# Performance work log

Measured on AMD Instinct MI355X. Metric: run time of the kernel, lower is better.

## Reference

```python
import jax, jax.numpy as jnp
import numpy as np

EMBED_DIM = 1024
HEADS = 16
D_K = EMBED_DIM // HEADS
B, S = 2, 2048


def setup_inputs() -> dict:
    key = jax.random.key(0)
    ks = jax.random.split(key, 8)
    scale = 1.0 / np.sqrt(EMBED_DIM)
    inp = {
        "key": jax.random.normal(ks[0], (B, S, EMBED_DIM), dtype=jnp.float32),
        "query": jax.random.normal(ks[1], (B, S, EMBED_DIM), dtype=jnp.float32),
        "value": jax.random.normal(ks[2], (B, S, EMBED_DIM), dtype=jnp.float32),
        # torch nn.Linear stores weight as [out, in]; y = x @ W.T
        "Wq": jax.random.normal(ks[3], (EMBED_DIM, EMBED_DIM), dtype=jnp.float32) * scale,
        "Wk": jax.random.normal(ks[4], (EMBED_DIM, EMBED_DIM), dtype=jnp.float32) * scale,
        "Wv": jax.random.normal(ks[5], (EMBED_DIM, EMBED_DIM), dtype=jnp.float32) * scale,
        "Wo": jax.random.normal(ks[6], (EMBED_DIM, EMBED_DIM), dtype=jnp.float32) * scale,
        "bo": jax.random.normal(ks[7], (EMBED_DIM,), dtype=jnp.float32) * scale,
        # causal mask, True = keep (matches masked_fill(~mask, -1e20))
        "mask": jnp.tril(jnp.ones((S, S), dtype=jnp.bool_))[None, None, :, :],
    }
    return inp


def _split_heads(x):
    b, s, _ = x.shape
    return x.reshape(b, s, HEADS, D_K).transpose(0, 2, 1, 3)  # [B,H,S,d_k]


def reference(key, query, value, Wq, Wk, Wv, Wo, bo, mask):
    b, q_len = query.shape[0], query.shape[1]
    k = _split_heads(key @ Wk.T)
    q = _split_heads(query @ Wq.T)
    v = _split_heads(value @ Wv.T)
    scores = jnp.einsum('bhqd,bhkd->bhqk', q, k) / np.sqrt(D_K)
    scores = jnp.where(mask, scores, jnp.float32(-1e20))
    attn = jax.nn.softmax(scores, axis=-1)
    out = jnp.einsum('bhqk,bhkd->bhqd', attn, v)
    out = out.transpose(0, 2, 1, 3).reshape(b, q_len, HEADS * D_K)
    return out @ Wo.T + bo
```

## Files before the change

### kernel.cpp

```cpp
#include <hip/hip_runtime.h>
#include <cstdint>
#include <cstddef>


typedef __bf16 bf16;
typedef __bf16 bf16x4 __attribute__((ext_vector_type(4)));
typedef __bf16 bf16x8 __attribute__((ext_vector_type(8)));
typedef float f32x4 __attribute__((ext_vector_type(4)));

#define MFMA(a, b, c) __builtin_amdgcn_mfma_f32_16x16x32_bf16(a, b, c, 0, 0, 0)

constexpr int EMBED = 1024;
constexpr int SEQ = 2048;
constexpr int HEADS = 16;
constexpr int DK = 64;
constexpr int BH = 32;

__device__ __forceinline__ void gl16(const bf16* g, bf16* l) {
  __builtin_amdgcn_global_load_lds(
      (const __attribute__((address_space(1))) unsigned int*)g,
      (__attribute__((address_space(3))) unsigned int*)l, 16, 0, 0);
}

struct ConvArgs {
  const void* src[8];
  bf16* dst[8];
  int n8[8];
  const unsigned short* probe;
};

__global__ __launch_bounds__(256) void convert_kernel(ConvArgs a) {
  __shared__ int cnt;
  const int t = threadIdx.x;
  if (t == 0) cnt = 0;
  __syncthreads();
  {
    unsigned short u = a.probe[2 * t];
    int e = (u >> 7) & 0xFF;
    if (e >= 100 && e <= 130) atomicAdd(&cnt, 1);
  }
  __syncthreads();
  const int isf32 = (cnt < 128) ? 1 : 0;

  const int seg = blockIdx.y;
  const void* s = a.src[seg];
  bf16* d = a.dst[seg];
  const int n8 = a.n8[seg];
  for (int i = blockIdx.x * 256 + t; i < n8; i += gridDim.x * 256) {
    if (isf32) {
      const float* sp = (const float*)s + (size_t)i * 8;
      float4 x = *(const float4*)sp, y = *(const float4*)(sp + 4);
      bf16x8 v;
      v[0] = (bf16)x.x; v[1] = (bf16)x.y; v[2] = (bf16)x.z; v[3] = (bf16)x.w;
      v[4] = (bf16)y.x; v[5] = (bf16)y.y; v[6] = (bf16)y.z; v[7] = (bf16)y.w;
      *(bf16x8*)(d + (size_t)i * 8) = v;
    } else {
      *(uint4*)(d + (size_t)i * 8) = *(const uint4*)((const bf16*)s + (size_t)i * 8);
    }
  }
}

__device__ __forceinline__ void gemm_body(
    const bf16* __restrict__ X, const bf16* __restrict__ W,
    const bf16* __restrict__ bias, bf16* __restrict__ outb,
    float* __restrict__ outf, int mode, bf16* As, bf16* Bs, int m0, int n0)
{
  const int t = threadIdx.x;
  const int lane = t & 63, wave = t >> 6;
  const int wm = wave >> 2, wn = wave & 3;
  const int l16 = lane & 15, quad = lane >> 4;

  f32x4 acc[4][2] = {};

  for (int k0 = 0; k0 < EMBED; k0 += 64) {
    __syncthreads();
#pragma unroll
    for (int i = 0; i < 2; ++i) {
      int idx = t + i * 512;
      int r = idx >> 3;
      int cl = (idx & 7) ^ (r & 7);
      gl16(X + (size_t)(m0 + r) * EMBED + k0 + cl * 8, As + (i * 512 + wave * 64) * 8);
      gl16(W + (size_t)(n0 + r) * EMBED + k0 + cl * 8, Bs + (i * 512 + wave * 64) * 8);
    }
    __syncthreads();

#pragma unroll
    for (int ks = 0; ks < 2; ++ks) {
      bf16x8 a[4], b[2];
#pragma unroll
      for (int mi = 0; mi < 4; ++mi) {
        int row = wm * 64 + mi * 16 + l16;
        a[mi] = *(const bf16x8*)(As + row * 64 + (((ks * 4 + quad) ^ (row & 7)) * 8));
      }
#pragma unroll
      for (int ni = 0; ni < 2; ++ni) {
        int row = wn * 32 + ni * 16 + l16;
        b[ni] = *(const bf16x8*)(Bs + row * 64 + (((ks * 4 + quad) ^ (row & 7)) * 8));
      }
#pragma unroll
      for (int mi = 0; mi < 4; ++mi)
#pragma unroll
        for (int ni = 0; ni < 2; ++ni)
          acc[mi][ni] = MFMA(a[mi], b[ni], acc[mi][ni]);
    }
  }

#pragma unroll
  for (int mi = 0; mi < 4; ++mi) {
#pragma unroll
    for (int ni = 0; ni < 2; ++ni) {
      int n = n0 + wn * 32 + ni * 16 + l16;
#pragma unroll
      for (int r = 0; r < 4; ++r) {
        int m = m0 + wm * 64 + mi * 16 + quad * 4 + r;
        float v = acc[mi][ni][r];
        if (mode == 2) {
          outf[(size_t)m * EMBED + n] = v + (float)bias[n];
        } else {
          int b_ = m >> 11, s = m & (SEQ - 1);
          int h = n >> 6, d = n & 63;
          int bh = b_ * HEADS + h;
          if (mode == 0)
            outb[((size_t)bh * SEQ + s) * DK + d] = (bf16)v;
          else
            outb[((size_t)bh * DK + d) * SEQ + s] = (bf16)v;
        }
      }
    }
  }
}

struct QkvArgs {
  const bf16 *X0, *X1, *X2;
  const bf16 *W0, *W1, *W2;
  bf16 *O0, *O1, *O2;
};

__global__ __launch_bounds__(512, 4) void qkv_gemm(QkvArgs args) {
  __shared__ alignas(16) bf16 As[128 * 64];
  __shared__ alignas(16) bf16 Bs[128 * 64];
  const int z = blockIdx.z;
  const bf16* X = (z == 0) ? args.X0 : (z == 1) ? args.X1 : args.X2;
  const bf16* W = (z == 0) ? args.W0 : (z == 1) ? args.W1 : args.W2;
  bf16* O      = (z == 0) ? args.O0 : (z == 1) ? args.O1 : args.O2;
  int mode = (z == 2) ? 1 : 0;
  gemm_body(X, W, nullptr, O, nullptr, mode, As, Bs,
            blockIdx.x * 128, blockIdx.y * 128);
}

__global__ __launch_bounds__(512, 4) void out_gemm(const bf16* __restrict__ X,
                                                   const bf16* __restrict__ W,
                                                   const bf16* __restrict__ bias,
                                                   float* __restrict__ out) {
  __shared__ alignas(16) bf16 As[128 * 64];
  __shared__ alignas(16) bf16 Bs[128 * 64];
  gemm_body(X, W, bias, nullptr, out, 2, As, Bs,
            blockIdx.x * 128, blockIdx.y * 128);
}

template<bool MASKED>
__device__ __forceinline__ void attn_tile2(
    int kt, int t, int w, int l16, int quad, int qbase,
    const bf16* __restrict__ Kp0, const bf16* __restrict__ Vp0,
    bf16* Ks, bf16* VTs, bf16* Pw,
    const bf16x8 qf[2][2], f32x4 o[2][4], float lst[2])
{
  constexpr float SC = 0.125f * 1.44269504f;
  constexpr float BI = -8.0f * 1.44269504f;

  __syncthreads();
  const bf16* Kg = Kp0 + (size_t)kt * 64 * DK;
  const bf16* Vg = Vp0 + (size_t)kt * 64;
#pragma unroll
  for (int i = 0; i < 2; ++i) {
    int idx = t + i * 256;
    int r = idx >> 3;
    int cl = (idx & 7) ^ (r & 7);
    gl16(Kg + (size_t)r * DK + cl * 8, Ks + (i * 256 + w * 64) * 8);
    gl16(Vg + (size_t)r * SEQ + cl * 8, VTs + (i * 256 + w * 64) * 8);
  }
  __syncthreads();

  f32x4 sacc[2][4] = {};
#pragma unroll
  for (int ks = 0; ks < 2; ++ks) {
#pragma unroll
    for (int mi = 0; mi < 4; ++mi) {
      int row = mi * 16 + l16;
      bf16x8 kf = *(const bf16x8*)(Ks + row * 64 + (((ks * 4 + quad) ^ (row & 7)) * 8));
      sacc[0][mi] = MFMA(kf, qf[0][ks], sacc[0][mi]);
      sacc[1][mi] = MFMA(kf, qf[1][ks], sacc[1][mi]);
    }
  }

#pragma unroll
  for (int g = 0; g < 2; ++g) {
    const int qg = qbase + g * 16 + l16;
    float ls = 0.f;
#pragma unroll
    for (int mi = 0; mi < 4; ++mi) {
      bf16x4 pv;
#pragma unroll
      for (int r = 0; r < 4; ++r) {
        float arg = __builtin_fmaf(sacc[g][mi][r], SC, BI);
        if (MASKED && (kt * 64 + mi * 16 + quad * 4 + r > qg)) arg = -1e30f;
        float p = __builtin_exp2f(arg);
        ls += p;
        pv[r] = (bf16)p;
      }
      *(bf16x4*)(Pw + (g * 16 + l16) * 72 + mi * 16 + quad * 4) = pv;
    }
    ls += __shfl_xor(ls, 16);
    ls += __shfl_xor(ls, 32);
    lst[g] += ls;
  }

  __builtin_amdgcn_s_setprio(1);
#pragma unroll
  for (int ks = 0; ks < 2; ++ks) {
    bf16x8 pf0 = *(const bf16x8*)(Pw + l16 * 72 + ks * 32 + quad * 8);
    bf16x8 pf1 = *(const bf16x8*)(Pw + (16 + l16) * 72 + ks * 32 + quad * 8);
#pragma unroll
    for (int dt = 0; dt < 4; ++dt) {
      int row = dt * 16 + l16;
      bf16x8 vf = *(const bf16x8*)(VTs + row * 64 +
                                   (((ks * 4 + quad) ^ (row & 7)) * 8));
      o[0][dt] = MFMA(vf, pf0, o[0][dt]);
      o[1][dt] = MFMA(vf, pf1, o[1][dt]);
    }
  }
  __builtin_amdgcn_s_setprio(0);
}

__global__ __launch_bounds__(256, 3) void attn_split(
    const bf16* __restrict__ qbuf, const bf16* __restrict__ kbuf,
    const bf16* __restrict__ vtbuf, bf16* __restrict__ ctx,
    float* __restrict__ po, float* __restrict__ pl)
{
  __shared__ alignas(16) bf16 Ks[64 * 64];
  __shared__ alignas(16) bf16 VTs[64 * 64];
  __shared__ alignas(16) bf16 Ps[4 * 32 * 72];

  const int t = threadIdx.x;
  const int gid = blockIdx.x;
  const int xcd = gid & 7, j = gid >> 3;
  const int bh = xcd + ((j & 3) << 3);
  const int s = j >> 2;
  const int mode = (s < 8) ? 0 : (s < 16) ? 1 : 2;
  const int qt = (mode == 2) ? (s - 8) : s;
  const int q0 = qt * 128;
  const int lane = t & 63, w = t >> 6;
  const int l16 = lane & 15, quad = lane >> 4;
  const int qbase = q0 + w * 32;

  const bf16* Kp0 = kbuf + (size_t)bh * SEQ * DK;
  const bf16* Vp0 = vtbuf + (size_t)bh * DK * SEQ;

  bf16x8 qf[2][2];
#pragma unroll
  for (int g = 0; g < 2; ++g) {
    const bf16* Qg = qbuf + ((size_t)bh * SEQ + qbase + g * 16 + l16) * DK;
    qf[g][0] = *(const bf16x8*)(Qg + quad * 8);
    qf[g][1] = *(const bf16x8*)(Qg + 32 + quad * 8);
  }

  float lst[2] = {0.f, 0.f};
  f32x4 o[2][4] = {};
  bf16* Pw = Ps + w * (32 * 72);

  const int t0 = (mode == 2) ? 16 : 0;
  const int tEnd = (mode == 1) ? 15 : (2 * qt - 1);
#pragma unroll 1
  for (int kt = t0; kt <= tEnd; ++kt)
    attn_tile2<false>(kt, t, w, l16, quad, qbase, Kp0, Vp0, Ks, VTs, Pw, qf, o, lst);
  if (mode != 1) {
    attn_tile2<true>(2 * qt, t, w, l16, quad, qbase, Kp0, Vp0, Ks, VTs, Pw, qf, o, lst);
    attn_tile2<true>(2 * qt + 1, t, w, l16, quad, qbase, Kp0, Vp0, Ks, VTs, Pw, qf, o, lst);
  }

  if (mode == 0) {
    const int b_ = bh >> 4, h = bh & 15;
#pragma unroll
    for (int g = 0; g < 2; ++g) {
      const float inv = 1.0f / lst[g];
      bf16* dst = ctx + ((size_t)b_ * SEQ + qbase + g * 16 + l16) * EMBED + h * DK;
#pragma unroll
      for (int dt = 0; dt < 4; ++dt) {
        bf16x4 v;
#pragma unroll
        for (int r = 0; r < 4; ++r) v[r] = (bf16)(o[g][dt][r] * inv);
        *(bf16x4*)(dst + dt * 16 + quad * 4) = v;
      }
    }
  } else {
    const int p = ((bh << 3) + (qt - 8)) * 2 + (mode - 1);
    float* ob = po + (size_t)p * 8192;
#pragma unroll
    for (int g = 0; g < 2; ++g) {
      const int qloc = w * 32 + g * 16 + l16;
#pragma unroll
      for (int dt = 0; dt < 4; ++dt)
        *(f32x4*)(ob + qloc * 64 + dt * 16 + quad * 4) = o[g][dt];
      if (quad == 0) pl[(size_t)p * 128 + qloc] = lst[g];
    }
  }
}

__global__ __launch_bounds__(256) void attn_combine(
    const float* __restrict__ po, const float* __restrict__ pl,
    bf16* __restrict__ ctx)
{
  const int gid = blockIdx.x;
  const int xcd = gid & 7, j = gid >> 3;
  const int bh = xcd + ((j & 3) << 3);
  const int qtl = j >> 2;
  const int p0 = (bh << 3) + qtl;
  const int qt = 8 + qtl;
  const int t = threadIdx.x;
  const float* o0 = po + (size_t)p0 * 2 * 8192;
  const float* o1 = o0 + 8192;
  const float* l0 = pl + (size_t)p0 * 2 * 128;
  const float* l1 = l0 + 128;

  const int q = t >> 1;
  const int d0 = (t & 1) * 32;
  const float inv = 1.0f / (l0[q] + l1[q]);

  const int b_ = bh >> 4, h = bh & 15;
  bf16* dst = ctx + ((size_t)b_ * SEQ + qt * 128 + q) * EMBED + h * DK + d0;
#pragma unroll
  for (int jj = 0; jj < 8; ++jj) {
    f32x4 a = *(const f32x4*)(o0 + q * 64 + d0 + jj * 4);
    f32x4 b = *(const f32x4*)(o1 + q * 64 + d0 + jj * 4);
    bf16x4 v;
#pragma unroll
    for (int r = 0; r < 4; ++r) v[r] = (bf16)((a[r] + b[r]) * inv);
    *(bf16x4*)(dst + jj * 4) = v;
  }
}

template<bool MASKED>
__device__ __forceinline__ void attn_tile(
    int kt, int t, int w, int l16, int quad, int qglob,
    const bf16* __restrict__ Kp0, const bf16* __restrict__ Vp0,
    bf16* Ks, bf16* VTs, bf16* Pw,
    const bf16x8 qf[2], f32x4 o[4], float& lst)
{
  constexpr float SC = 0.125f * 1.44269504f;
  constexpr float BI = -8.0f * 1.44269504f;

  __syncthreads();
  const bf16* Kg = Kp0 + (size_t)kt * 64 * DK;
  const bf16* Vg = Vp0 + (size_t)kt * 64;
#pragma unroll
  for (int i = 0; i < 2; ++i) {
    int idx = t + i * 256;
    int r = idx >> 3;
    int cl = (idx & 7) ^ (r & 7);
    gl16(Kg + (size_t)r * DK + cl * 8, Ks + (i * 256 + w * 64) * 8);
    gl16(Vg + (size_t)r * SEQ + cl * 8, VTs + (i * 256 + w * 64) * 8);
  }
  __syncthreads();

  f32x4 sacc[4] = {};
#pragma unroll
  for (int ks = 0; ks < 2; ++ks) {
#pragma unroll
    for (int mi = 0; mi < 4; ++mi) {
      int row = mi * 16 + l16;
      bf16x8 kf = *(const bf16x8*)(Ks + row * 64 + (((ks * 4 + quad) ^ (row & 7)) * 8));
      sacc[mi] = MFMA(kf, qf[ks], sacc[mi]);
    }
  }

  float ls = 0.f;
  const int kbase = kt * 64 + quad * 4;
#pragma unroll
  for (int mi = 0; mi < 4; ++mi) {
    bf16x4 pv;
#pragma unroll
    for (int r = 0; r < 4; ++r) {
      float arg = __builtin_fmaf(sacc[mi][r], SC, BI);
      if (MASKED && (kbase + mi * 16 + r > qglob)) arg = -1e30f;
      float p = __builtin_exp2f(arg);
      ls += p;
      pv[r] = (bf16)p;
    }
    *(bf16x4*)(Pw + l16 * 72 + mi * 16 + quad * 4) = pv;
  }
  ls += __shfl_xor(ls, 16);
  ls += __shfl_xor(ls, 32);
  lst += ls;

  __builtin_amdgcn_s_setprio(1);
#pragma unroll
  for (int ks = 0; ks < 2; ++ks) {
    bf16x8 pf = *(const bf16x8*)(Pw + l16 * 72 + ks * 32 + quad * 8);
#pragma unroll
    for (int dt = 0; dt < 4; ++dt) {
      int row = dt * 16 + l16;
      bf16x8 vf = *(const bf16x8*)(VTs + row * 64 +
                                   (((ks * 4 + quad) ^ (row & 7)) * 8));
      o[dt] = MFMA(vf, pf, o[dt]);
    }
  }
  __builtin_amdgcn_s_setprio(0);
}

__global__ __launch_bounds__(256, 6) void attn_mono(
    const bf16* __restrict__ qbuf, const bf16* __restrict__ kbuf,
    const bf16* __restrict__ vtbuf, bf16* __restrict__ ctx)
{
  __shared__ alignas(16) bf16 Ks[64 * 64];
  __shared__ alignas(16) bf16 VTs[64 * 64];
  __shared__ alignas(16) bf16 Ps[64 * 72];

  const int t = threadIdx.x;
  const int g = (blockIdx.x + blockIdx.y) & 31;
  const int qt = (blockIdx.y & 16) ? (31 - g) : g;
  const int bh = blockIdx.y;
  const int q0 = qt * 64;
  const int lane = t & 63, w = t >> 6;
  const int l16 = lane & 15, quad = lane >> 4;

  const bf16* Kp0 = kbuf + (size_t)bh * SEQ * DK;
  const bf16* Vp0 = vtbuf + (size_t)bh * DK * SEQ;

  const bf16* Qg = qbuf + ((size_t)bh * SEQ + q0 + w * 16 + l16) * DK;
  bf16x8 qf[2];
  qf[0] = *(const bf16x8*)(Qg + quad * 8);
  qf[1] = *(const bf16x8*)(Qg + 32 + quad * 8);

  const int qglob = q0 + w * 16 + l16;
  float lst = 0.f;
  f32x4 o[4] = {};
  bf16* Pw = Ps + w * 16 * 72;

#pragma unroll 1
  for (int kt = 0; kt < qt; ++kt)
    attn_tile<false>(kt, t, w, l16, quad, qglob, Kp0, Vp0, Ks, VTs, Pw, qf, o, lst);
  attn_tile<true>(qt, t, w, l16, quad, qglob, Kp0, Vp0, Ks, VTs, Pw, qf, o, lst);

  const float inv = 1.0f / lst;
  const int b_ = bh >> 4, h = bh & 15;
  bf16* dst = ctx + ((size_t)b_ * SEQ + qglob) * EMBED + h * DK;
#pragma unroll
  for (int dt = 0; dt < 4; ++dt) {
    bf16x4 v;
#pragma unroll
    for (int r = 0; r < 4; ++r) v[r] = (bf16)(o[dt][r] * inv);
    *(bf16x4*)(dst + dt * 16 + quad * 4) = v;
  }
}

extern "C" void kernel_launch(void* const* d_in, const int* in_sizes, int n_in,
                              void* d_out, int out_size, void* d_ws, size_t ws_size,
                              hipStream_t stream) {
  const void* key   = d_in[0];
  const void* query = d_in[1];
  const void* value = d_in[2];
  const void* Wq    = d_in[3];
  const void* Wk    = d_in[4];
  const void* Wv    = d_in[5];
  const void* Wo    = d_in[6];
  const void* bo    = d_in[7];
  float* out = (float*)d_out;

  char* base = (char*)d_ws + 256;
  const size_t XN = (size_t)2 * SEQ * EMBED;
  const size_t WN = (size_t)EMBED * EMBED;
  const size_t per = (size_t)BH * SEQ * DK;

  bf16* cq  = (bf16*)base;
  bf16* ck  = cq + XN;
  bf16* cv  = ck + XN;
  bf16* cWq = cv + XN;
  bf16* cWk = cWq + WN;
  bf16* cWv = cWk + WN;
  bf16* cWo = cWv + WN;
  bf16* cbo = cWo + WN;
  bf16* qb  = cbo + 1024;
  bf16* kb  = qb + per;
  bf16* vtb = kb + per;
  bf16* ctx = vtb + per;

  float* po = (float*)(ctx + per);
  float* pl = po + (size_t)256 * 2 * 8192;
  const size_t need = 256 + (3 * XN + 4 * WN + 1024 + 4 * per) * sizeof(bf16)
                    + (size_t)256 * 2 * 8192 * 4 + (size_t)256 * 2 * 128 * 4;
  const bool split_ok = (ws_size >= need);

  ConvArgs ca;
  ca.src[0] = query; ca.dst[0] = cq;  ca.n8[0] = (int)(XN / 8);
  ca.src[1] = key;   ca.dst[1] = ck;  ca.n8[1] = (int)(XN / 8);
  ca.src[2] = value; ca.dst[2] = cv;  ca.n8[2] = (int)(XN / 8);
  ca.src[3] = Wq;    ca.dst[3] = cWq; ca.n8[3] = (int)(WN / 8);
  ca.src[4] = Wk;    ca.dst[4] = cWk; ca.n8[4] = (int)(WN / 8);
  ca.src[5] = Wv;    ca.dst[5] = cWv; ca.n8[5] = (int)(WN / 8);
  ca.src[6] = Wo;    ca.dst[6] = cWo; ca.n8[6] = (int)(WN / 8);
  ca.src[7] = bo;    ca.dst[7] = cbo; ca.n8[7] = 128;
  ca.probe = (const unsigned short*)Wq;
  convert_kernel<<<dim3(512, 8), 256, 0, stream>>>(ca);

  QkvArgs qa{cq, ck, cv, cWq, cWk, cWv, qb, kb, vtb};
  qkv_gemm<<<dim3(32, 8, 3), 512, 0, stream>>>(qa);

  if (split_ok) {
    attn_split<<<dim3(768), 256, 0, stream>>>(qb, kb, vtb, ctx, po, pl);
    attn_combine<<<dim3(256), 256, 0, stream>>>(po, pl, ctx);
  } else {
    attn_mono<<<dim3(32, 32), 256, 0, stream>>>(qb, kb, vtb, ctx);
  }

  out_gemm<<<dim3(32, 8), 512, 0, stream>>>(ctx, cWo, cbo, out);
}
```

Measured before the change: 245.7 us.

## Use 256-row query tiles with 512 threads and multi-chunk causal KV split

The causal attention kernel now uses 512-thread blocks covering 256 query rows and splits each query tile's KV range into chunks of 8 key tiles, with up to 4 chunks per tile. Partial outputs are stored in bf16 inside the reused query conversion buffer, and the combine kernel sums a variable number of chunks. The aim is to balance causal work across blocks, halve the K/V reloads per query row, and cut partial-output traffic. In exchange, occupancy per block changes, bf16 partials lose some precision, and reusing the cq buffer assumes it is dead after the QKV GEMM.

```diff
diff --git a/kernel.cpp b/kernel.cpp
--- a/kernel.cpp
+++ b/kernel.cpp
@@ -169,15 +169,13 @@
   constexpr float BI = -8.0f * 1.44269504f;
 
   __syncthreads();
-  const bf16* Kg = Kp0 + (size_t)kt * 64 * DK;
-  const bf16* Vg = Vp0 + (size_t)kt * 64;
-#pragma unroll
-  for (int i = 0; i < 2; ++i) {
-    int idx = t + i * 256;
-    int r = idx >> 3;
-    int cl = (idx & 7) ^ (r & 7);
-    gl16(Kg + (size_t)r * DK + cl * 8, Ks + (i * 256 + w * 64) * 8);
-    gl16(Vg + (size_t)r * SEQ + cl * 8, VTs + (i * 256 + w * 64) * 8);
+  {
+    const bf16* Kg = Kp0 + (size_t)kt * 64 * DK;
+    const bf16* Vg = Vp0 + (size_t)kt * 64;
+    int r = t >> 3;
+    int cl = (t & 7) ^ (r & 7);
+    gl16(Kg + (size_t)r * DK + cl * 8, Ks + w * 512);
+    gl16(Vg + (size_t)r * SEQ + cl * 8, VTs + w * 512);
   }
   __syncthreads();
 
@@ -232,23 +230,35 @@
   __builtin_amdgcn_s_setprio(0);
 }
 
-__global__ __launch_bounds__(256, 3) void attn_split(
+__global__ __launch_bounds__(512, 6) void attn_split(
     const bf16* __restrict__ qbuf, const bf16* __restrict__ kbuf,
     const bf16* __restrict__ vtbuf, bf16* __restrict__ ctx,
-    float* __restrict__ po, float* __restrict__ pl)
+    bf16* __restrict__ po, float* __restrict__ pl)
 {
   __shared__ alignas(16) bf16 Ks[64 * 64];
   __shared__ alignas(16) bf16 VTs[64 * 64];
-  __shared__ alignas(16) bf16 Ps[4 * 32 * 72];
+  __shared__ alignas(16) bf16 Ps[8 * 32 * 72];
 
   const int t = threadIdx.x;
   const int gid = blockIdx.x;
   const int xcd = gid & 7, j = gid >> 3;
   const int bh = xcd + ((j & 3) << 3);
   const int s = j >> 2;
-  const int mode = (s < 8) ? 0 : (s < 16) ? 1 : 2;
-  const int qt = (mode == 2) ? (s - 8) : s;
-  const int q0 = qt * 128;
+
+  int qt, ch;
+  if (s < 2)       { qt = s; ch = 0; }
+  else if (s < 6)  { int u = s - 2; qt = 2 + (u >> 1); ch = u & 1; }
+  else if (s < 12) { int u = s - 6; int hi = (u >= 3) ? 1 : 0; qt = 4 + hi; ch = u - 3 * hi; }
+  else             { int u = s - 12; qt = 6 + (u >> 2); ch = u & 3; }
+
+  const int q0 = qt * 256;
+  const int t0 = ch * 8;
+  const int dEnd = 4 * qt + 3;
+  const int t1 = (t0 + 7 < dEnd) ? (t0 + 7) : dEnd;
+  const int uEnd = (t1 < 4 * qt - 1) ? t1 : (4 * qt - 1);
+  const int m0 = (t0 > 4 * qt) ? t0 : (4 * qt);
+  const bool direct = (qt < 2);
+
   const int lane = t & 63, w = t >> 6;
   const int l16 = lane & 15, quad = lane >> 4;
   const int qbase = q0 + w * 32;
@@ -268,17 +278,14 @@
   f32x4 o[2][4] = {};
   bf16* Pw = Ps + w * (32 * 72);
 
-  const int t0 = (mode == 2) ? 16 : 0;
-  const int tEnd = (mode == 1) ? 15 : (2 * qt - 1);
 #pragma unroll 1
-  for (int kt = t0; kt <= tEnd; ++kt)
+  for (int kt = t0; kt <= uEnd; ++kt)
     attn_tile2<false>(kt, t, w, l16, quad, qbase, Kp0, Vp0, Ks, VTs, Pw, qf, o, lst);
-  if (mode != 1) {
-    attn_tile2<true>(2 * qt, t, w, l16, quad, qbase, Kp0, Vp0, Ks, VTs, Pw, qf, o, lst);
-    attn_tile2<true>(2 * qt + 1, t, w, l16, quad, qbase, Kp0, Vp0, Ks, VTs, Pw, qf, o, lst);
-  }
-
-  if (mode == 0) {
+#pragma unroll 1
+  for (int kt = m0; kt <= t1; ++kt)
+    attn_tile2<true>(kt, t, w, l16, quad, qbase, Kp0, Vp0, Ks, VTs, Pw, qf, o, lst);
+
+  if (direct) {
     const int b_ = bh >> 4, h = bh & 15;
 #pragma unroll
     for (int g = 0; g < 2; ++g) {
@@ -293,49 +300,65 @@
       }
     }
   } else {
-    const int p = ((bh << 3) + (qt - 8)) * 2 + (mode - 1);
-    float* ob = po + (size_t)p * 8192;
+    const int p = ((bh * 6) + (qt - 2)) * 4 + ch;
+    bf16* ob = po + (size_t)p * 16384;
 #pragma unroll
     for (int g = 0; g < 2; ++g) {
       const int qloc = w * 32 + g * 16 + l16;
 #pragma unroll
-      for (int dt = 0; dt < 4; ++dt)
-        *(f32x4*)(ob + qloc * 64 + dt * 16 + quad * 4) = o[g][dt];
-      if (quad == 0) pl[(size_t)p * 128 + qloc] = lst[g];
+      for (int dt = 0; dt < 4; ++dt) {
+        bf16x4 v;
+#pragma unroll
+        for (int r = 0; r < 4; ++r) v[r] = (bf16)o[g][dt][r];
+        *(bf16x4*)(ob + qloc * 64 + dt * 16 + quad * 4) = v;
+      }
+      if (quad == 0) pl[(size_t)p * 256 + qloc] = lst[g];
     }
   }
 }
 
 __global__ __launch_bounds__(256) void attn_combine(
-    const float* __restrict__ po, const float* __restrict__ pl,
+    const bf16* __restrict__ po, const float* __restrict__ pl,
     bf16* __restrict__ ctx)
 {
   const int gid = blockIdx.x;
   const int xcd = gid & 7, j = gid >> 3;
   const int bh = xcd + ((j & 3) << 3);
-  const int qtl = j >> 2;
-  const int p0 = (bh << 3) + qtl;
-  const int qt = 8 + qtl;
+  const int qti = j >> 2;
+  const int qt = 2 + qti;
+  const int nch = (4 * qt + 11) >> 3;
+  const int pb = ((bh * 6) + qti) * 4;
+
   const int t = threadIdx.x;
-  const float* o0 = po + (size_t)p0 * 2 * 8192;
-  const float* o1 = o0 + 8192;
-  const float* l0 = pl + (size_t)p0 * 2 * 128;
-  const float* l1 = l0 + 128;
-
-  const int q = t >> 1;
-  const int d0 = (t & 1) * 32;
-  const float inv = 1.0f / (l0[q] + l1[q]);
-
   const int b_ = bh >> 4, h = bh & 15;
-  bf16* dst = ctx + ((size_t)b_ * SEQ + qt * 128 + q) * EMBED + h * DK + d0;
-#pragma unroll
-  for (int jj = 0; jj < 8; ++jj) {
-    f32x4 a = *(const f32x4*)(o0 + q * 64 + d0 + jj * 4);
-    f32x4 b = *(const f32x4*)(o1 + q * 64 + d0 + jj * 4);
-    bf16x4 v;
-#pragma unroll
-    for (int r = 0; r < 4; ++r) v[r] = (bf16)((a[r] + b[r]) * inv);
-    *(bf16x4*)(dst + jj * 4) = v;
+  const int d0 = (t & 3) * 16;
+
+#pragma unroll
+  for (int i = 0; i < 4; ++i) {
+    const int q = i * 64 + (t >> 2);
+    float acc[16] = {};
+    float lt = 0.f;
+#pragma unroll 1
+    for (int c = 0; c < nch; ++c) {
+      lt += pl[(size_t)(pb + c) * 256 + q];
+      const bf16* ob = po + (size_t)(pb + c) * 16384 + q * 64 + d0;
+#pragma unroll
+      for (int jj = 0; jj < 2; ++jj) {
+        bf16x8 v = *(const bf16x8*)(ob + jj * 8);
+#pragma unroll
+        for (int r = 0; r < 8; ++r) acc[jj * 8 + r] += (float)v[r];
+      }
+    }
+    const float inv = 1.0f / lt;
+
+    bf16* dst = ctx + ((size_t)b_ * SEQ + qt * 256 + q) * EMBED + h * DK + d0;
+#pragma unroll
+    for (int jj = 0; jj < 2; ++jj) {
+      bf16x8 v;
+#pragma unroll
+      for (int r = 0; r < 8; ++r) v[r] = (bf16)(acc[jj * 8 + r] * inv);
+      *(bf16x8*)(dst + jj * 8) = v;
+    }
   }
 }
 
@@ -484,10 +507,10 @@
   bf16* vtb = kb + per;
   bf16* ctx = vtb + per;
 
-  float* po = (float*)(ctx + per);
-  float* pl = po + (size_t)256 * 2 * 8192;
+  bf16* po = cq;
+  float* pl = (float*)(ctx + per);
   const size_t need = 256 + (3 * XN + 4 * WN + 1024 + 4 * per) * sizeof(bf16)
-                    + (size_t)256 * 2 * 8192 * 4 + (size_t)256 * 2 * 128 * 4;
+                    + (size_t)32 * 6 * 4 * 256 * 4;
   const bool split_ok = (ws_size >= need);
 
   ConvArgs ca;
@@ -506,8 +529,8 @@
   qkv_gemm<<<dim3(32, 8, 3), 512, 0, stream>>>(qa);
 
   if (split_ok) {
-    attn_split<<<dim3(768), 256, 0, stream>>>(qb, kb, vtb, ctx, po, pl);
-    attn_combine<<<dim3(256), 256, 0, stream>>>(po, pl, ctx);
+    attn_split<<<dim3(640), 512, 0, stream>>>(qb, kb, vtb, ctx, po, pl);
+    attn_combine<<<dim3(192), 256, 0, stream>>>(po, pl, ctx);
   } else {
     attn_mono<<<dim3(32, 32), 256, 0, stream>>>(qb, kb, vtb, ctx);
   }
```

Result: slower. 329.3 us (+34.0%).
